# Kernel tuning notes

Hardware: AMD Instinct MI355X
Metric: run time of the kernel (lower is better)

The kernel has to match this reference:

```python
import jax, jax.numpy as jnp
import numpy as np

UNITS = 1024
NUM_HEADS = 16
MAX_DIST = 20  # hardcoded default in RelativePositionalEmbedding
SEQ = 41       # forced: 2*MAX_DIST+1 must broadcast against S
DIN = 41       # forced: embedding last dim must broadcast against S
BATCH = 2048


def setup_inputs() -> dict:
    key = jax.random.key(0)
    ks = jax.random.split(key, 12)
    g = lambda k, shape, fan: jax.random.normal(k, shape, jnp.float32) * (1.0 / np.sqrt(fan))
    return {
        "x": jax.random.normal(ks[0], (BATCH, SEQ, DIN), jnp.float32),
        "Wq": g(ks[1], (DIN, UNITS), DIN), "bq": jnp.zeros((UNITS,), jnp.float32),
        "Wk": g(ks[2], (DIN, UNITS), DIN), "bk": jnp.zeros((UNITS,), jnp.float32),
        "Wv": g(ks[3], (DIN, UNITS), DIN), "bv": jnp.zeros((UNITS,), jnp.float32),
        "Wo": g(ks[4], (UNITS, UNITS), UNITS), "bo": jnp.zeros((UNITS,), jnp.float32),
        "rel_emb": g(ks[5], (2 * MAX_DIST + 1, DIN), DIN),  # (41, 41)
    }


def _split_heads(t):  # (B,S,U) -> (B,H,S,dh)
    B, S, U = t.shape
    return t.reshape(B, S, NUM_HEADS, U // NUM_HEADS).transpose(0, 2, 1, 3)


def reference(x, Wq, bq, Wk, bk, Wv, bv, Wo, bo, rel_emb):
    B, S, _ = x.shape
    q = _split_heads(x @ Wq + bq)
    k = _split_heads(x @ Wk + bk)
    v = _split_heads(x @ Wv + bv)
    dh = q.shape[-1]
    scores = jnp.einsum("bhsd,bhtd->bhst", q, k) / jnp.sqrt(jnp.float32(dh))
    # relative positional bias: gather with clipped indices (identity here since MAX_DIST < S)
    idx = jnp.clip(jnp.arange(-MAX_DIST, MAX_DIST + 1), -S + 1, S - 1) + MAX_DIST
    pos = rel_emb[idx]                      # (2*MAX_DIST+1, DIN) == (S, S)
    scores = scores + pos[None, None]       # broadcast over (B,H)
    attn = jax.nn.softmax(scores, axis=-1)
    out = jnp.einsum("bhst,bhtd->bhsd", attn, v)
    out = out.transpose(0, 2, 1, 3).reshape(B, S, UNITS)
    return out @ Wo + bo
```

## Files before the change

### kernel.cpp

```cpp
#include <hip/hip_runtime.h>
#include <hip/hip_bf16.h>

typedef __attribute__((ext_vector_type(8))) short s16x8;
typedef __attribute__((ext_vector_type(4))) float f32x4;

#define MFMA16(a, b, c) __builtin_amdgcn_mfma_f32_16x16x32_bf16((a), (b), (c), 0, 0, 0)

__device__ __forceinline__ short f2bf(float f) {
    union { float f; unsigned u; } v; v.f = f;
    unsigned r = v.u + 0x7FFFu + ((v.u >> 16) & 1u);
    return (short)(r >> 16);
}

__global__ void prep_weights(const float* __restrict__ Wq, const float* __restrict__ Wk,
                             const float* __restrict__ Wv, const float* __restrict__ Wo,
                             short* __restrict__ WqkvT, short* __restrict__ WoT) {
    int i = blockIdx.x * 256 + threadIdx.x;
    const int T1 = 3 * 1024 * 64;
    if (i < T1) {
        int kk = i & 63, n = (i >> 6) & 1023, m = i >> 16;
        const float* W = (m == 0) ? Wq : ((m == 1) ? Wk : Wv);
        float v = (kk < 41) ? W[kk * 1024 + n] : 0.f;
        WqkvT[i] = f2bf(v);
    } else {
        int j = i - T1;
        int kk = j & 1023, n = j >> 10;
        WoT[j] = f2bf(Wo[kk * 1024 + n]);
    }
}

#define SP 48
#define PADW 72

__global__ __launch_bounds__(256) void attn_kernel(
    const float* __restrict__ x, const float* __restrict__ bq,
    const float* __restrict__ bk, const float* __restrict__ bv,
    const float* __restrict__ rel, const short* __restrict__ WqkvT,
    float* __restrict__ out)
{
    __shared__ short xs[SP][PADW];
    __shared__ short qs[SP][PADW];
    __shared__ short ks_[SP][PADW];
    __shared__ short vsT[64][PADW];
    __shared__ short ps[SP][PADW];
    __shared__ float ss[SP][49];

    int b = blockIdx.x >> 4, h = blockIdx.x & 15;
    int tid = threadIdx.x;
    int lane = tid & 63, wave = tid >> 6;
    int l15 = lane & 15, l4 = lane >> 4;

    const float* xb = x + (size_t)b * (41 * 41);
    for (int idx = tid; idx < SP * 64; idx += 256) {
        int r = idx >> 6, c = idx & 63;
        float v = (r < 41 && c < 41) ? xb[r * 41 + c] : 0.f;
        xs[r][c] = f2bf(v);
    }
    for (int idx = tid; idx < 64 * 16; idx += 256) {
        int d = idx >> 4, t = 48 + (idx & 15);
        vsT[d][t] = 0;
    }
    __syncthreads();

    for (int t = wave; t < 36; t += 4) {
        int mat = t / 12, sub = t % 12, mt = sub >> 2, nt = sub & 3;
        f32x4 acc = {0.f, 0.f, 0.f, 0.f};
        const short* wbase = WqkvT + ((size_t)(mat * 1024 + h * 64 + nt * 16 + l15)) * 64 + l4 * 8;
        const short* abase = &xs[mt * 16 + l15][l4 * 8];
#pragma unroll
        for (int ksi = 0; ksi < 2; ++ksi) {
            s16x8 a = *(const s16x8*)(abase + ksi * 32);
            s16x8 bb = *(const s16x8*)(wbase + ksi * 32);
            acc = MFMA16(a, bb, acc);
        }
        const float* bias = (mat == 0) ? bq : ((mat == 1) ? bk : bv);
        float bval = bias[h * 64 + nt * 16 + l15];
        float scale = (mat == 0) ? 0.125f : 1.0f;
#pragma unroll
        for (int i = 0; i < 4; ++i) {
            int row = mt * 16 + l4 * 4 + i;
            int col = nt * 16 + l15;
            short v = f2bf((acc[i] + bval) * scale);
            if (mat == 0) qs[row][col] = v;
            else if (mat == 1) ks_[row][col] = v;
            else vsT[col][row] = v;
        }
    }
    __syncthreads();

    for (int t = wave; t < 9; t += 4) {
        int mt = t / 3, nt = t % 3;
        f32x4 acc = {0.f, 0.f, 0.f, 0.f};
#pragma unroll
        for (int ksi = 0; ksi < 2; ++ksi) {
            s16x8 a = *(const s16x8*)(&qs[mt * 16 + l15][ksi * 32 + l4 * 8]);
            s16x8 bb = *(const s16x8*)(&ks_[nt * 16 + l15][ksi * 32 + l4 * 8]);
            acc = MFMA16(a, bb, acc);
        }
#pragma unroll
        for (int i = 0; i < 4; ++i)
            ss[mt * 16 + l4 * 4 + i][nt * 16 + l15] = acc[i];
    }
    __syncthreads();

    if (tid < SP) {
        int r = tid;
        int rr = (r < 41) ? r : 40;
        const float* relrow = rel + rr * 41;
        float m = -1e30f;
        for (int c = 0; c < 41; ++c) {
            float s = ss[r][c] + relrow[c];
            ss[r][c] = s;
            m = fmaxf(m, s);
        }
        float sum = 0.f;
        for (int c = 0; c < 41; ++c) {
            float e = __expf(ss[r][c] - m);
            ss[r][c] = e;
            sum += e;
        }
        float inv = 1.f / sum;
        for (int c = 0; c < 41; ++c) ps[r][c] = f2bf(ss[r][c] * inv);
        for (int c = 41; c < 64; ++c) ps[r][c] = 0;
    }
    __syncthreads();

    for (int t = wave; t < 12; t += 4) {
        int mt = t / 4, nt = t % 4;
        f32x4 acc = {0.f, 0.f, 0.f, 0.f};
#pragma unroll
        for (int ksi = 0; ksi < 2; ++ksi) {
            s16x8 a = *(const s16x8*)(&ps[mt * 16 + l15][ksi * 32 + l4 * 8]);
            s16x8 bb = *(const s16x8*)(&vsT[nt * 16 + l15][ksi * 32 + l4 * 8]);
            acc = MFMA16(a, bb, acc);
        }
#pragma unroll
        for (int i = 0; i < 4; ++i) {
            int s = mt * 16 + l4 * 4 + i;
            if (s < 41)
                out[((size_t)b * 41 + s) * 1024 + h * 64 + nt * 16 + l15] = acc[i];
        }
    }
}

__global__ __launch_bounds__(512) void proj_kernel(
    float* __restrict__ io, const short* __restrict__ WoT,
    const float* __restrict__ bo)
{
    __shared__ short As[2][64][40];

    int m0 = blockIdx.x * 64;
    int tid = threadIdx.x;
    int lane = tid & 63, wave = tid >> 6;
    int l15 = lane & 15, l4 = lane >> 4;

    int srow = tid >> 3;
    int scol = (tid & 7) * 4;

    f32x4 acc[4][8];
#pragma unroll
    for (int mt = 0; mt < 4; ++mt)
#pragma unroll
        for (int nt = 0; nt < 8; ++nt) acc[mt][nt] = (f32x4){0.f, 0.f, 0.f, 0.f};

    const float* arow = io + (size_t)(m0 + srow) * 1024 + scol;

    {
        f32x4 v = *(const f32x4*)(arow);
        union { short s[4]; unsigned long long u; } pk;
#pragma unroll
        for (int i = 0; i < 4; ++i) pk.s[i] = f2bf(v[i]);
        *(unsigned long long*)&As[0][srow][scol] = pk.u;
    }
    __syncthreads();

    for (int kk = 0; kk < 32; ++kk) {
        int cur = kk & 1;
        f32x4 nxt;
        bool have = (kk + 1 < 32);
        if (have) nxt = *(const f32x4*)(arow + (kk + 1) * 32);

        s16x8 afr[4];
#pragma unroll
        for (int mt = 0; mt < 4; ++mt)
            afr[mt] = *(const s16x8*)(&As[cur][mt * 16 + l15][l4 * 8]);
        s16x8 bfr[8];
#pragma unroll
        for (int nt = 0; nt < 8; ++nt) {
            const short* wb = WoT + (size_t)(wave * 128 + nt * 16 + l15) * 1024 + kk * 32 + l4 * 8;
            bfr[nt] = *(const s16x8*)wb;
        }
#pragma unroll
        for (int nt = 0; nt < 8; ++nt)
#pragma unroll
            for (int mt = 0; mt < 4; ++mt)
                acc[mt][nt] = MFMA16(afr[mt], bfr[nt], acc[mt][nt]);

        __syncthreads();
        if (have) {
            union { short s[4]; unsigned long long u; } pk;
#pragma unroll
            for (int i = 0; i < 4; ++i) pk.s[i] = f2bf(nxt[i]);
            *(unsigned long long*)&As[cur ^ 1][srow][scol] = pk.u;
        }
        __syncthreads();
    }

#pragma unroll
    for (int nt = 0; nt < 8; ++nt) {
        int col = wave * 128 + nt * 16 + l15;
        float bb = bo[col];
#pragma unroll
        for (int mt = 0; mt < 4; ++mt) {
#pragma unroll
            for (int i = 0; i < 4; ++i) {
                int row = m0 + mt * 16 + l4 * 4 + i;
                io[(size_t)row * 1024 + col] = acc[mt][nt][i] + bb;
            }
        }
    }
}

extern "C" void kernel_launch(void* const* d_in, const int* in_sizes, int n_in,
                              void* d_out, int out_size, void* d_ws, size_t ws_size,
                              hipStream_t stream) {
    const float* x   = (const float*)d_in[0];
    const float* Wq  = (const float*)d_in[1];
    const float* bq  = (const float*)d_in[2];
    const float* Wk  = (const float*)d_in[3];
    const float* bk  = (const float*)d_in[4];
    const float* Wv  = (const float*)d_in[5];
    const float* bv  = (const float*)d_in[6];
    const float* Wo  = (const float*)d_in[7];
    const float* bo  = (const float*)d_in[8];
    const float* rel = (const float*)d_in[9];

    short* WqkvT = (short*)d_ws;
    short* WoT   = WqkvT + 3 * 1024 * 64;
    float* out   = (float*)d_out;

    hipLaunchKernelGGL(prep_weights, dim3(4864), dim3(256), 0, stream,
                       Wq, Wk, Wv, Wo, WqkvT, WoT);
    hipLaunchKernelGGL(attn_kernel, dim3(2048 * 16), dim3(256), 0, stream,
                       x, bq, bk, bv, rel, WqkvT, out);
    hipLaunchKernelGGL(proj_kernel, dim3(83968 / 64), dim3(512), 0, stream,
                       out, WoT, bo);
}
```

Before: 1.426 ms.

## Stage attention output in bf16 workspace and retile output projection

The attention kernel can now write its output as bf16 into a workspace buffer, and a new projection kernel reads that buffer. The new kernel uses 64x256 tiles, a 64-wide K step and an XOR-swizzled LDS layout. Softmax is spread across all waves with 16-lane shuffle reductions, and the relative bias is added during the score store. The weight prep kernel now transposes through shared memory so its reads and writes are coalesced. The bf16 path only runs when the workspace is large enough (about 172MB); otherwise the old fp32 path is used.

```diff
diff --git a/kernel.cpp b/kernel.cpp
--- a/kernel.cpp
+++ b/kernel.cpp
@@ -12,38 +12,63 @@
     return (short)(r >> 16);
 }
 
-__global__ void prep_weights(const float* __restrict__ Wq, const float* __restrict__ Wk,
-                             const float* __restrict__ Wv, const float* __restrict__ Wo,
-                             short* __restrict__ WqkvT, short* __restrict__ WoT) {
-    int i = blockIdx.x * 256 + threadIdx.x;
-    const int T1 = 3 * 1024 * 64;
-    if (i < T1) {
-        int kk = i & 63, n = (i >> 6) & 1023, m = i >> 16;
-        const float* W = (m == 0) ? Wq : ((m == 1) ? Wk : Wv);
-        float v = (kk < 41) ? W[kk * 1024 + n] : 0.f;
-        WqkvT[i] = f2bf(v);
+__global__ __launch_bounds__(256) void prep_weights(
+    const float* __restrict__ Wq, const float* __restrict__ Wk,
+    const float* __restrict__ Wv, const float* __restrict__ Wo,
+    short* __restrict__ WqkvT, short* __restrict__ WoT)
+{
+    __shared__ short sh[64][73];
+
+    int blk = blockIdx.x;
+    const float* W; short* out; int K, Kp, k0, n0;
+    if (blk < 48) {
+        int m = blk >> 4, ntile = blk & 15;
+        W = (m == 0) ? Wq : ((m == 1) ? Wk : Wv);
+        out = WqkvT + m * 1024 * 64;
+        K = 41; Kp = 64; k0 = 0; n0 = ntile * 64;
     } else {
-        int j = i - T1;
-        int kk = j & 1023, n = j >> 10;
-        WoT[j] = f2bf(Wo[kk * 1024 + n]);
+        int t = blk - 48;
+        W = Wo; out = WoT; K = 1024; Kp = 1024;
+        k0 = (t >> 4) * 64; n0 = (t & 15) * 64;
+    }
+    int tid = threadIdx.x;
+#pragma unroll
+    for (int p = 0; p < 16; ++p) {
+        int kk = p * 4 + (tid >> 6);
+        int nn = tid & 63;
+        int k = k0 + kk;
+        float v = (k < K) ? W[(size_t)k * 1024 + n0 + nn] : 0.f;
+        sh[kk][nn] = f2bf(v);
+    }
+    __syncthreads();
+#pragma unroll
+    for (int p = 0; p < 2; ++p) {
+        int nn = p * 32 + (tid >> 3);
+        int kk8 = (tid & 7) * 8;
+        union { short s[8]; s16x8 v; } pk;
+#pragma unroll
+        for (int j = 0; j < 8; ++j) pk.s[j] = sh[kk8 + j][nn];
+        *(s16x8*)&out[(size_t)(n0 + nn) * Kp + k0 + kk8] = pk.v;
     }
 }
 
 #define SP 48
 #define PADW 72
 
+template<bool TOBF>
 __global__ __launch_bounds__(256) void attn_kernel(
     const float* __restrict__ x, const float* __restrict__ bq,
     const float* __restrict__ bk, const float* __restrict__ bv,
     const float* __restrict__ rel, const short* __restrict__ WqkvT,
-    float* __restrict__ out)
+    void* __restrict__ outp)
 {
     __shared__ short xs[SP][PADW];
     __shared__ short qs[SP][PADW];
     __shared__ short ks_[SP][PADW];
     __shared__ short vsT[64][PADW];
-    __shared__ short ps[SP][PADW];
-    __shared__ float ss[SP][49];
+    __shared__ float ss[SP][48];
+
+    short (*ps)[PADW] = xs;
 
     int b = blockIdx.x >> 4, h = blockIdx.x & 15;
     int tid = threadIdx.x;
@@ -56,10 +81,8 @@
         float v = (r < 41 && c < 41) ? xb[r * 41 + c] : 0.f;
         xs[r][c] = f2bf(v);
     }
-    for (int idx = tid; idx < 64 * 16; idx += 256) {
-        int d = idx >> 4, t = 48 + (idx & 15);
-        vsT[d][t] = 0;
-    }
+    for (int idx = tid; idx < 64 * 16; idx += 256)
+        vsT[idx >> 4][48 + (idx & 15)] = 0;
     __syncthreads();
 
     for (int t = wave; t < 36; t += 4) {
@@ -98,30 +121,36 @@
             acc = MFMA16(a, bb, acc);
         }
 #pragma unroll
-        for (int i = 0; i < 4; ++i)
-            ss[mt * 16 + l4 * 4 + i][nt * 16 + l15] = acc[i];
-    }
-    __syncthreads();
-
-    if (tid < SP) {
-        int r = tid;
-        int rr = (r < 41) ? r : 40;
-        const float* relrow = rel + rr * 41;
-        float m = -1e30f;
-        for (int c = 0; c < 41; ++c) {
-            float s = ss[r][c] + relrow[c];
-            ss[r][c] = s;
-            m = fmaxf(m, s);
-        }
-        float sum = 0.f;
-        for (int c = 0; c < 41; ++c) {
-            float e = __expf(ss[r][c] - m);
-            ss[r][c] = e;
-            sum += e;
-        }
-        float inv = 1.f / sum;
-        for (int c = 0; c < 41; ++c) ps[r][c] = f2bf(ss[r][c] * inv);
-        for (int c = 41; c < 64; ++c) ps[r][c] = 0;
+        for (int i = 0; i < 4; ++i) {
+            int row = mt * 16 + l4 * 4 + i;
+            int col = nt * 16 + l15;
+            int rr = (row < 41) ? row : 40;
+            float rv = (col < 41) ? rel[rr * 41 + col] : 0.f;
+            ss[row][col] = acc[i] + rv;
+        }
+    }
+    __syncthreads();
+
+#pragma unroll
+    for (int p = 0; p < 3; ++p) {
+        int r = wave * 4 + p * 16 + l4;
+        float v0 = ss[r][l15];
+        float v1 = ss[r][l15 + 16];
+        bool has2 = (l15 < 9);
+        float v2 = has2 ? ss[r][l15 + 32] : -3.0e38f;
+        float m = fmaxf(fmaxf(v0, v1), v2);
+#pragma unroll
+        for (int off = 8; off; off >>= 1) m = fmaxf(m, __shfl_xor(m, off, 16));
+        float e0 = __expf(v0 - m), e1 = __expf(v1 - m);
+        float e2 = has2 ? __expf(v2 - m) : 0.f;
+        float s = e0 + e1 + e2;
+#pragma unroll
+        for (int off = 8; off; off >>= 1) s += __shfl_xor(s, off, 16);
+        float inv = 1.f / s;
+        ps[r][l15]      = f2bf(e0 * inv);
+        ps[r][l15 + 16] = f2bf(e1 * inv);
+        ps[r][l15 + 32] = has2 ? f2bf(e2 * inv) : (short)0;
+        ps[r][l15 + 48] = 0;
     }
     __syncthreads();
 
@@ -137,13 +166,99 @@
 #pragma unroll
         for (int i = 0; i < 4; ++i) {
             int s = mt * 16 + l4 * 4 + i;
-            if (s < 41)
-                out[((size_t)b * 41 + s) * 1024 + h * 64 + nt * 16 + l15] = acc[i];
-        }
-    }
-}
-
-__global__ __launch_bounds__(512) void proj_kernel(
+            if (s < 41) {
+                size_t off = ((size_t)b * 41 + s) * 1024 + h * 64 + nt * 16 + l15;
+                if (TOBF) ((short*)outp)[off] = f2bf(acc[i]);
+                else      ((float*)outp)[off] = acc[i];
+            }
+        }
+    }
+}
+
+__global__ __launch_bounds__(256) void proj_a(
+    const short* __restrict__ Ab, float* __restrict__ out,
+    const short* __restrict__ WoT, const float* __restrict__ bo)
+{
+    __shared__ short As[2][64 * 64];
+
+    int m0 = (blockIdx.x >> 2) * 64;
+    int n0 = (blockIdx.x & 3) * 256;
+    int tid = threadIdx.x, lane = tid & 63, wave = tid >> 6;
+    int l15 = lane & 15, l4 = lane >> 4;
+
+    f32x4 acc[4][4];
+#pragma unroll
+    for (int mt = 0; mt < 4; ++mt)
+#pragma unroll
+        for (int nt = 0; nt < 4; ++nt) acc[mt][nt] = (f32x4){0.f, 0.f, 0.f, 0.f};
+
+    int srow = tid >> 2;
+    int part = tid & 3;
+    const short* asrc = Ab + (size_t)(m0 + srow) * 1024 + part * 16;
+    int u0 = (2 * part) ^ (srow & 7);
+    int u1 = (2 * part + 1) ^ (srow & 7);
+    int d0 = srow * 64 + u0 * 8;
+    int d1 = srow * 64 + u1 * 8;
+
+    {
+        s16x8 r0 = *(const s16x8*)(asrc);
+        s16x8 r1 = *(const s16x8*)(asrc + 8);
+        *(s16x8*)&As[0][d0] = r0;
+        *(s16x8*)&As[0][d1] = r1;
+    }
+    __syncthreads();
+
+    const short* wbase = WoT + (size_t)(n0 + wave * 64) * 1024;
+
+    for (int kt = 0; kt < 16; ++kt) {
+        int cur = kt & 1;
+        s16x8 nr0, nr1;
+        bool have = (kt < 15);
+        if (have) {
+            const short* s = asrc + (kt + 1) * 64;
+            nr0 = *(const s16x8*)(s);
+            nr1 = *(const s16x8*)(s + 8);
+        }
+#pragma unroll
+        for (int ksi = 0; ksi < 2; ++ksi) {
+            s16x8 afr[4], bfr[4];
+#pragma unroll
+            for (int mt = 0; mt < 4; ++mt) {
+                int row = mt * 16 + l15;
+                int u = (ksi * 4 + l4) ^ (row & 7);
+                afr[mt] = *(const s16x8*)&As[cur][row * 64 + u * 8];
+            }
+#pragma unroll
+            for (int nt = 0; nt < 4; ++nt)
+                bfr[nt] = *(const s16x8*)(wbase + (size_t)(nt * 16 + l15) * 1024
+                                          + kt * 64 + ksi * 32 + l4 * 8);
+#pragma unroll
+            for (int nt = 0; nt < 4; ++nt)
+#pragma unroll
+                for (int mt = 0; mt < 4; ++mt)
+                    acc[mt][nt] = MFMA16(afr[mt], bfr[nt], acc[mt][nt]);
+        }
+        __syncthreads();
+        if (have) {
+            *(s16x8*)&As[cur ^ 1][d0] = nr0;
+            *(s16x8*)&As[cur ^ 1][d1] = nr1;
+        }
+        __syncthreads();
+    }
+
+#pragma unroll
+    for (int nt = 0; nt < 4; ++nt) {
+        int col = n0 + wave * 64 + nt * 16 + l15;
+        float bb = bo[col];
+#pragma unroll
+        for (int mt = 0; mt < 4; ++mt)
+#pragma unroll
+            for (int i = 0; i < 4; ++i)
+                out[(size_t)(m0 + mt * 16 + l4 * 4 + i) * 1024 + col] = acc[mt][nt][i] + bb;
+    }
+}
+
+__global__ __launch_bounds__(512) void proj_b(
     float* __restrict__ io, const short* __restrict__ WoT,
     const float* __restrict__ bo)
 {
@@ -153,7 +268,6 @@
     int tid = threadIdx.x;
     int lane = tid & 63, wave = tid >> 6;
     int l15 = lane & 15, l4 = lane >> 4;
-
     int srow = tid >> 3;
     int scol = (tid & 7) * 4;
 
@@ -164,7 +278,6 @@
         for (int nt = 0; nt < 8; ++nt) acc[mt][nt] = (f32x4){0.f, 0.f, 0.f, 0.f};
 
     const float* arow = io + (size_t)(m0 + srow) * 1024 + scol;
-
     {
         f32x4 v = *(const f32x4*)(arow);
         union { short s[4]; unsigned long long u; } pk;
@@ -186,10 +299,9 @@
             afr[mt] = *(const s16x8*)(&As[cur][mt * 16 + l15][l4 * 8]);
         s16x8 bfr[8];
 #pragma unroll
-        for (int nt = 0; nt < 8; ++nt) {
-            const short* wb = WoT + (size_t)(wave * 128 + nt * 16 + l15) * 1024 + kk * 32 + l4 * 8;
-            bfr[nt] = *(const s16x8*)wb;
-        }
+        for (int nt = 0; nt < 8; ++nt)
+            bfr[nt] = *(const s16x8*)(WoT + (size_t)(wave * 128 + nt * 16 + l15) * 1024
+                                      + kk * 32 + l4 * 8);
 #pragma unroll
         for (int nt = 0; nt < 8; ++nt)
 #pragma unroll
@@ -211,13 +323,10 @@
         int col = wave * 128 + nt * 16 + l15;
         float bb = bo[col];
 #pragma unroll
-        for (int mt = 0; mt < 4; ++mt) {
-#pragma unroll
-            for (int i = 0; i < 4; ++i) {
-                int row = m0 + mt * 16 + l4 * 4 + i;
-                io[(size_t)row * 1024 + col] = acc[mt][nt][i] + bb;
-            }
-        }
+        for (int mt = 0; mt < 4; ++mt)
+#pragma unroll
+            for (int i = 0; i < 4; ++i)
+                io[(size_t)(m0 + mt * 16 + l4 * 4 + i) * 1024 + col] = acc[mt][nt][i] + bb;
     }
 }
 
@@ -237,12 +346,24 @@
 
     short* WqkvT = (short*)d_ws;
     short* WoT   = WqkvT + 3 * 1024 * 64;
+    short* Abf   = WoT + 1024 * 1024;
     float* out   = (float*)d_out;
 
-    hipLaunchKernelGGL(prep_weights, dim3(4864), dim3(256), 0, stream,
+    const size_t ABF_BYTES = (size_t)83968 * 1024 * 2;
+    const size_t W_BYTES   = (3 * 1024 * 64 + 1024 * 1024) * sizeof(short);
+    bool bigws = ws_size >= W_BYTES + ABF_BYTES;
+
+    hipLaunchKernelGGL(prep_weights, dim3(304), dim3(256), 0, stream,
                        Wq, Wk, Wv, Wo, WqkvT, WoT);
-    hipLaunchKernelGGL(attn_kernel, dim3(2048 * 16), dim3(256), 0, stream,
-                       x, bq, bk, bv, rel, WqkvT, out);
-    hipLaunchKernelGGL(proj_kernel, dim3(83968 / 64), dim3(512), 0, stream,
-                       out, WoT, bo);
-}
+    if (bigws) {
+        hipLaunchKernelGGL((attn_kernel<true>), dim3(2048 * 16), dim3(256), 0, stream,
+                           x, bq, bk, bv, rel, WqkvT, (void*)Abf);
+        hipLaunchKernelGGL(proj_a, dim3(1312 * 4), dim3(256), 0, stream,
+                           Abf, out, WoT, bo);
+    } else {
+        hipLaunchKernelGGL((attn_kernel<false>), dim3(2048 * 16), dim3(256), 0, stream,
+                           x, bq, bk, bv, rel, WqkvT, (void*)out);
+        hipLaunchKernelGGL(proj_b, dim3(83968 / 64), dim3(512), 0, stream,
+                           out, WoT, bo);
+    }
+}
```

Measured after the change: 1.306 ms. -8.5%, faster.
